# Performance work log

Hardware: AMD Instinct MI355X
Metric: run time of the kernel (lower is better)

Reference implementation:

```python
import jax, jax.numpy as jnp
import numpy as np

RADIUS = 3       # corr_radius
NUM_LEVELS = 4   # corr_lvls


def avg_pool2(x):
    """2x2 avg-pool with stride 2 on the last two axes (floor semantics, like F.avg_pool2d)."""
    nd = x.ndim
    s = jax.lax.reduce_window(
        x, 0.0, jax.lax.add,
        window_dimensions=(1,) * (nd - 2) + (2, 2),
        window_strides=(1,) * (nd - 2) + (2, 2),
        padding='VALID')
    return s * 0.25


def bilinear_window_lookup(corr, coords, radius):
    """corr: [B,H,W,hl,wl] per-pixel correlation maps; coords: [B,H,W,2] (x,y) in
    level-pixel units. Samples a (2r+1)^2 window around each coord with bilinear
    interpolation and zero padding (matches grid_sample align_corners=True, zeros).
    Returns [B,H,W,(2r+1)^2]."""
    B, H, W, hl, wl = corr.shape
    r = radius
    d = jnp.arange(-r, r + 1, dtype=coords.dtype)
    dy, dx = jnp.meshgrid(d, d, indexing='ij')
    delta = jnp.stack([dx.ravel(), dy.ravel()], axis=-1)        # [K2,2] (x,y)
    pts = coords[:, :, :, None, :] + delta                       # [B,H,W,K2,2]
    x, y = pts[..., 0], pts[..., 1]
    x0 = jnp.floor(x); y0 = jnp.floor(y)
    x1 = x0 + 1.0;     y1 = y0 + 1.0
    wx1 = x - x0; wx0 = 1.0 - wx1
    wy1 = y - y0; wy0 = 1.0 - wy1
    bi = jnp.arange(B)[:, None, None, None]
    hi = jnp.arange(H)[None, :, None, None]
    wi = jnp.arange(W)[None, None, :, None]

    def gather(xc, yc):
        valid = (xc >= 0) & (xc <= wl - 1) & (yc >= 0) & (yc <= hl - 1)
        xi = jnp.clip(xc, 0, wl - 1).astype(jnp.int32)
        yi = jnp.clip(yc, 0, hl - 1).astype(jnp.int32)
        return corr[bi, hi, wi, yi, xi] * valid.astype(corr.dtype)

    return (gather(x0, y0) * wx0 * wy0 + gather(x1, y0) * wx1 * wy0 +
            gather(x0, y1) * wx0 * wy1 + gather(x1, y1) * wx1 * wy1)


def pyramid_lookup(pyr, coords, radius):
    """pyr: list of [B,H,W,hl,wl]; coords: [B,H,W,2] at full level-0 resolution.
    Returns [B, L*(2r+1)^2, H, W]."""
    outs = [bilinear_window_lookup(c, coords / float(2 ** lvl), radius)
            for lvl, c in enumerate(pyr)]
    out = jnp.concatenate(outs, axis=-1)
    return jnp.transpose(out, (0, 3, 1, 2))


def setup_inputs() -> dict:
    key = jax.random.key(0)
    k0, k1, k2, k3, k4 = jax.random.split(key, 5)
    B, D, H, W = 1, 128, 60, 108  # 1/8-res features of a padded 480x864 frame
    fmap0 = jax.random.normal(k0, (B, D, H, W), dtype=jnp.float32)
    fmap1 = jax.random.normal(k1, (B, D, H, W), dtype=jnp.float32)
    flow0 = jax.random.normal(k2, (B, 2, H, W), dtype=jnp.float32)
    flow1 = jax.random.normal(k3, (B, 2, H, W), dtype=jnp.float32)
    embt = jax.random.uniform(k4, (B, 1, 1, 1), dtype=jnp.float32,
                              minval=0.1, maxval=0.9)
    return {"fmap0": fmap0, "fmap1": fmap1, "flow0": flow0,
            "flow1": flow1, "embt": embt}


def reference(fmap0, fmap1, flow0, flow1, embt):
    """BidirCorrBlock construction + AMT._corr_scale_lookup (downsample=1).
    Returns [B, 2*L*(2r+1)^2 + 4, H, W]: bidirectional multi-level correlation
    features concatenated with the stacked flows (corr, flow of the torch code)."""
    B, D, H, W = fmap0.shape
    # all-pairs correlation volume, scaled by 1/sqrt(D) as in RAFT's CorrBlock
    corr = jnp.einsum('bchw,bcuv->bhwuv', fmap0, fmap1) / jnp.sqrt(
        jnp.asarray(D, fmap0.dtype))                       # [B,H,W,H,W]
    corr_T = jnp.transpose(corr, (0, 3, 4, 1, 2))          # reversed direction
    pyr, pyr_T = [corr], [corr_T]
    for _ in range(NUM_LEVELS - 1):
        pyr.append(avg_pool2(pyr[-1]))
        pyr_T.append(avg_pool2(pyr_T[-1]))

    # coords_grid: channels (x, y)
    ys, xs = jnp.meshgrid(jnp.arange(H, dtype=fmap0.dtype),
                          jnp.arange(W, dtype=fmap0.dtype), indexing='ij')
    coord = jnp.broadcast_to(jnp.stack([xs, ys], axis=-1), (B, H, W, 2))

    t1_scale = 1.0 / embt           # [B,1,1,1]
    t0_scale = 1.0 / (1.0 - embt)
    f0 = jnp.transpose(flow0, (0, 2, 3, 1))  # [B,H,W,2]
    f1 = jnp.transpose(flow1, (0, 2, 3, 1))
    coords0 = coord + f1 * t1_scale          # lookup args of corr_fn(...)
    coords1 = coord + f0 * t0_scale

    corr0 = pyramid_lookup(pyr, coords0, RADIUS)     # [B, L*K2, H, W]
    corr1 = pyramid_lookup(pyr_T, coords1, RADIUS)
    corr_out = jnp.concatenate([corr0, corr1], axis=1)
    flow_out = jnp.concatenate([flow0, flow1], axis=1)
    return jnp.concatenate([corr_out, flow_out], axis=1)
```

## Files before the change

### kernel.cpp

```cpp
#include <hip/hip_runtime.h>

typedef _Float16 h16;
typedef __attribute__((ext_vector_type(2))) h16 h2v;
typedef __attribute__((ext_vector_type(8))) h16 h8v;

constexpr int H_ = 60, W_ = 108, HW_ = 6480;

constexpr unsigned B_F0T  = 0;
constexpr unsigned B_F1T  = 1658880;
constexpr unsigned B_F0L1 = 3317760;
constexpr unsigned B_F0L2 = 3732480;
constexpr unsigned B_F0L3 = 3836160;
constexpr unsigned B_F1L1 = 3859456;
constexpr unsigned B_F1L2 = 4274176;
constexpr unsigned B_F1L3 = 4377856;

__global__ __launch_bounds__(256) void k_transpose(const float* __restrict__ f0,
                                                   const float* __restrict__ f1,
                                                   h16* __restrict__ ws) {
    __shared__ float lds[64 * 129];
    const float* src = blockIdx.y ? f1 : f0;
    h16* dst = (h16*)((char*)ws + (blockIdx.y ? B_F1T : B_F0T));
    const int p0 = blockIdx.x * 64;
    const int t  = threadIdx.x;
    const int pr = t & 63, cr = t >> 6;
    #pragma unroll
    for (int cb = 0; cb < 128; cb += 4) {
        int c = cb + cr, p = p0 + pr;
        if (p < HW_) lds[pr * 129 + c] = src[(size_t)c * HW_ + p];
    }
    __syncthreads();
    const int cw = t & 63, pw = t >> 6;
    #pragma unroll
    for (int pb = 0; pb < 64; pb += 4) {
        int p = p0 + pb + pw;
        if (p < HW_) {
            float a = lds[(pb + pw) * 129 + 2 * cw];
            float b = lds[(pb + pw) * 129 + 2 * cw + 1];
            h2v v; v.x = (h16)a; v.y = (h16)b;
            ((h2v*)dst)[(size_t)p * 64 + cw] = v;
        }
    }
}

__global__ __launch_bounds__(256) void k_pool(h16* __restrict__ wsh,
                                              int win, int hout, int wout,
                                              unsigned iA, unsigned oA,
                                              unsigned iB, unsigned oB) {
    char* ws = (char*)wsh;
    const unsigned off_in  = blockIdx.y ? iB : iA;
    const unsigned off_out = blockIdx.y ? oB : oA;
    const int idx = blockIdx.x * 256 + threadIdx.x;
    const int total = hout * wout * 16;
    if (idx >= total) return;
    const int pos = idx >> 4, q = idx & 15;
    const int y = pos / wout, x = pos - y * wout;
    const char* r0 = ws + off_in + (unsigned)(2 * y * win + 2 * x) * 256;
    const char* r2 = ws + off_in + (unsigned)((2 * y + 1) * win + 2 * x) * 256;
    h8v a = *(const h8v*)(r0 + q * 16);
    h8v b = *(const h8v*)(r0 + 256 + q * 16);
    h8v c = *(const h8v*)(r2 + q * 16);
    h8v d = *(const h8v*)(r2 + 256 + q * 16);
    h8v o;
    #pragma unroll
    for (int j = 0; j < 8; ++j)
        o[j] = (h16)((((float)a[j] + (float)b[j]) + ((float)c[j] + (float)d[j])) * 0.25f);
    *(h8v*)(ws + off_out + (unsigned)pos * 256 + q * 16) = o;
}

template <int CTRL>
__device__ __forceinline__ float dpp_add(float x) {
    int y = __builtin_amdgcn_update_dpp(0, __builtin_bit_cast(int, x),
                                        CTRL, 0xF, 0xF, true);
    return x + __builtin_bit_cast(float, y);
}

__device__ __forceinline__ float dot_u4(uint4 u, uint4 s, float acc) {
    acc = __builtin_amdgcn_fdot2(__builtin_bit_cast(h2v, u.x),
                                 __builtin_bit_cast(h2v, s.x), acc, false);
    acc = __builtin_amdgcn_fdot2(__builtin_bit_cast(h2v, u.y),
                                 __builtin_bit_cast(h2v, s.y), acc, false);
    acc = __builtin_amdgcn_fdot2(__builtin_bit_cast(h2v, u.z),
                                 __builtin_bit_cast(h2v, s.z), acc, false);
    acc = __builtin_amdgcn_fdot2(__builtin_bit_cast(h2v, u.w),
                                 __builtin_bit_cast(h2v, s.w), acc, false);
    return acc;
}

__global__ __launch_bounds__(256, 4) void k_lookup(const h16* __restrict__ wsh,
                                                   const float* __restrict__ flow0,
                                                   const float* __restrict__ flow1,
                                                   const float* __restrict__ embt,
                                                   float* __restrict__ out) {
    __shared__ float so[196][5];
    const char* ws = (const char*)wsh;
    const int bid = blockIdx.x;
    const int xcd = bid & 7;
    const int dir = xcd >> 2;
    const int ord = (xcd & 3) * 405 + (bid >> 3);
    const int pix0 = ord * 4;
    const int t = threadIdx.x;
    const int L = t & 63;
    const int pix = pix0 + (t >> 6);
    const int h = pix / 108, w = pix - h * 108;

    const float e = embt[0];
    const float scale = dir ? 1.0f / (1.0f - e) : 1.0f / e;
    const float* fl = dir ? flow0 : flow1;
    const float cx = (float)w + fl[pix] * scale;
    const float cy = (float)h + fl[HW_ + pix] * scale;

    const int ch = L & 7;
    const int p  = L >> 3;

    const unsigned sbase = (dir ? B_F1T : B_F0T) + (unsigned)pix * 256;
    uint4 su0 = *(const uint4*)(ws + sbase + ch * 16);
    uint4 su1 = *(const uint4*)(ws + sbase + 128 + ch * 16);
    {
        h8v a = __builtin_bit_cast(h8v, su0), b = __builtin_bit_cast(h8v, su1);
        #pragma unroll
        for (int k = 0; k < 8; ++k) {
            a[k] = a[k] * (h16)0.08838834764831845f;
            b[k] = b[k] * (h16)0.08838834764831845f;
        }
        su0 = __builtin_bit_cast(uint4, a);
        su1 = __builtin_bit_cast(uint4, b);
    }

    constexpr unsigned g0[4] = {B_F1T, B_F1L1, B_F1L2, B_F1L3};
    constexpr unsigned g1[4] = {B_F0T, B_F0L1, B_F0L2, B_F0L3};

    #pragma unroll
    for (int lvl = 0; lvl < 4; ++lvl) {
        const unsigned gbase = dir ? g1[lvl] : g0[lvl];
        const int wl = 108 >> lvl, hl = 60 >> lvl;
        const float inv = (lvl == 0) ? 1.f : (lvl == 1) ? 0.5f : (lvl == 2) ? 0.25f : 0.125f;
        const float cxl = cx * inv, cyl = cy * inv;
        const float bxf = floorf(cxl), byf = floorf(cyl);
        const int bx = (int)bxf, by = (int)byf;
        const int gx = bx - 3 + p;
        const int gxc = min(max(gx, 0), wl - 1);
        const bool colv = (gx >= 0) & (gx < wl);
        const int gyo = by - 3 + ch;
        const bool ownv = colv & (gyo >= 0) & (gyo < hl);

        const unsigned coloff = gbase + (unsigned)gxc * 256 + (unsigned)ch * 16;
        uint4 u0[8], u1[8];
        #pragma unroll
        for (int j = 0; j < 8; ++j) {
            const int gy = by - 3 + j;
            const int gyc = min(max(gy, 0), hl - 1);
            const unsigned ro = coloff + (unsigned)(gyc * wl) * 256;
            u0[j] = *(const uint4*)(ws + ro);
            u1[j] = *(const uint4*)(ws + ro + 128);
        }

        float dval = 0.0f;
        #pragma unroll
        for (int j = 0; j < 8; ++j) {
            float a0 = dot_u4(u0[j], su0, 0.0f);
            float a1 = dot_u4(u1[j], su1, 0.0f);
            float acc = a0 + a1;
            acc = dpp_add<0xB1>(acc);
            acc = dpp_add<0x4E>(acc);
            acc = dpp_add<0x141>(acc);
            dval = (ch == j) ? acc : dval;
        }
        dval = ownv ? dval : 0.0f;

        const int dyi = L / 7, dxi = L - dyi * 7;
        const float fx = cxl - bxf, fy = cyl - byf;
        const float d00 = __shfl(dval, 8 * dxi + dyi);
        const float d01 = __shfl(dval, 8 * dxi + dyi + 8);
        const float d10 = __shfl(dval, 8 * dxi + dyi + 1);
        const float d11 = __shfl(dval, 8 * dxi + dyi + 9);
        const float v = (d00 * (1.0f - fx) + d01 * fx) * (1.0f - fy) +
                        (d10 * (1.0f - fx) + d11 * fx) * fy;
        if (L < 49) so[lvl * 49 + L][t >> 6] = v;
    }
    __syncthreads();

    if (t < 196) {
        float4 o = make_float4(so[t][0], so[t][1], so[t][2], so[t][3]);
        *(float4*)(out + (size_t)(dir * 196 + t) * HW_ + pix0) = o;
    } else if (dir == 0 && t < 200) {
        const int c = t - 196;
        const float* f = (c < 2) ? flow0 + (size_t)c * HW_
                                 : flow1 + (size_t)(c - 2) * HW_;
        *(float4*)(out + (size_t)(392 + c) * HW_ + pix0) = *(const float4*)(f + pix0);
    }
}

extern "C" void kernel_launch(void* const* d_in, const int* in_sizes, int n_in,
                              void* d_out, int out_size, void* d_ws, size_t ws_size,
                              hipStream_t stream) {
    const float* fmap0 = (const float*)d_in[0];
    const float* fmap1 = (const float*)d_in[1];
    const float* flow0 = (const float*)d_in[2];
    const float* flow1 = (const float*)d_in[3];
    const float* embt  = (const float*)d_in[4];
    h16* ws  = (h16*)d_ws;
    float* out = (float*)d_out;

    k_transpose<<<dim3(102, 2), 256, 0, stream>>>(fmap0, fmap1, ws);
    k_pool<<<dim3(102, 2), 256, 0, stream>>>(ws, 108, 30, 54, B_F0T,  B_F0L1, B_F1T,  B_F1L1);
    k_pool<<<dim3(26, 2),  256, 0, stream>>>(ws,  54, 15, 27, B_F0L1, B_F0L2, B_F1L1, B_F1L2);
    k_pool<<<dim3(6, 2),   256, 0, stream>>>(ws,  27,  7, 13, B_F0L2, B_F0L3, B_F1L2, B_F1L3);
    k_lookup<<<dim3(405 * 8), 256, 0, stream>>>(ws, flow0, flow1, embt, out);
}
```

Baseline: 47.55 us.

## Fuse three pooling launches into one kernel computing all pyramid levels from level 0

Replaces the three sequential pooling kernels with a single launch whose block ranges compute levels 1, 2 and 3 directly from the full-resolution transposed features, using 4x4 and 8x8 averages. This removes two kernel launches and the serial dependency between levels. The cost is redundant reads of level 0 for the coarser levels. Averaging in float before a single rounding changes the numerics slightly compared with chained fp16 pooling.

New measurement: 44.62 us. -6.2%, faster.

```diff
diff --git a/kernel.cpp b/kernel.cpp
--- a/kernel.cpp
+++ b/kernel.cpp
@@ -43,29 +43,77 @@
     }
 }
 
-__global__ __launch_bounds__(256) void k_pool(h16* __restrict__ wsh,
-                                              int win, int hout, int wout,
-                                              unsigned iA, unsigned oA,
-                                              unsigned iB, unsigned oB) {
+__global__ __launch_bounds__(256) void k_pyramid(h16* __restrict__ wsh) {
     char* ws = (char*)wsh;
-    const unsigned off_in  = blockIdx.y ? iB : iA;
-    const unsigned off_out = blockIdx.y ? oB : oA;
-    const int idx = blockIdx.x * 256 + threadIdx.x;
-    const int total = hout * wout * 16;
-    if (idx >= total) return;
-    const int pos = idx >> 4, q = idx & 15;
-    const int y = pos / wout, x = pos - y * wout;
-    const char* r0 = ws + off_in + (unsigned)(2 * y * win + 2 * x) * 256;
-    const char* r2 = ws + off_in + (unsigned)((2 * y + 1) * win + 2 * x) * 256;
-    h8v a = *(const h8v*)(r0 + q * 16);
-    h8v b = *(const h8v*)(r0 + 256 + q * 16);
-    h8v c = *(const h8v*)(r2 + q * 16);
-    h8v d = *(const h8v*)(r2 + 256 + q * 16);
-    h8v o;
-    #pragma unroll
-    for (int j = 0; j < 8; ++j)
-        o[j] = (h16)((((float)a[j] + (float)b[j]) + ((float)c[j] + (float)d[j])) * 0.25f);
-    *(h8v*)(ws + off_out + (unsigned)pos * 256 + q * 16) = o;
+    const int map = blockIdx.y;
+    const unsigned srcB = map ? B_F1T : B_F0T;
+    const char* s = ws + srcB;
+    const int bid = blockIdx.x;
+    const int t = threadIdx.x;
+
+    if (bid < 102) {
+        const int idx = bid * 256 + t;
+        if (idx >= 1620 * 16) return;
+        const int pos = idx >> 4, q = idx & 15;
+        const int y = pos / 54, x = pos - y * 54;
+        const unsigned r0 = (unsigned)(2 * y * 108 + 2 * x) * 256 + q * 16;
+        const unsigned r1 = r0 + 108 * 256;
+        h8v a = *(const h8v*)(s + r0);
+        h8v b = *(const h8v*)(s + r0 + 256);
+        h8v c = *(const h8v*)(s + r1);
+        h8v d = *(const h8v*)(s + r1 + 256);
+        h8v o;
+        #pragma unroll
+        for (int k = 0; k < 8; ++k)
+            o[k] = (h16)((((float)a[k] + (float)b[k]) + ((float)c[k] + (float)d[k])) * 0.25f);
+        *(h8v*)(ws + (map ? B_F1L1 : B_F0L1) + (unsigned)pos * 256 + q * 16) = o;
+    } else if (bid < 128) {
+        const int idx = (bid - 102) * 256 + t;
+        if (idx >= 405 * 16) return;
+        const int pos = idx >> 4, q = idx & 15;
+        const int y = pos / 27, x = pos - y * 27;
+        float acc[8] = {};
+        #pragma unroll
+        for (int dy = 0; dy < 4; ++dy) {
+            #pragma unroll
+            for (int dx = 0; dx < 4; ++dx) {
+                h8v u = *(const h8v*)(s + (unsigned)((4 * y + dy) * 108 + 4 * x + dx) * 256 + q * 16);
+                #pragma unroll
+                for (int k = 0; k < 8; ++k) acc[k] += (float)u[k];
+            }
+        }
+        h8v o;
+        #pragma unroll
+        for (int k = 0; k < 8; ++k) o[k] = (h16)(acc[k] * 0.0625f);
+        *(h8v*)(ws + (map ? B_F1L2 : B_F0L2) + (unsigned)pos * 256 + q * 16) = o;
+    } else {
+        const int idx = (bid - 128) * 256 + t;
+        if (idx >= 91 * 128) return;
+        const int pos = idx >> 7;
+        const int sub = idx & 127;
+        const int half = sub >> 6, lane = sub & 63;
+        const int j = lane >> 3, qq = (lane & 7) + half * 8;
+        const int y = pos / 13, x = pos - y * 13;
+        float acc[8] = {};
+        #pragma unroll
+        for (int dx = 0; dx < 8; ++dx) {
+            h8v u = *(const h8v*)(s + (unsigned)((8 * y + j) * 108 + 8 * x + dx) * 256 + qq * 16);
+            #pragma unroll
+            for (int k = 0; k < 8; ++k) acc[k] += (float)u[k];
+        }
+        #pragma unroll
+        for (int k = 0; k < 8; ++k) {
+            acc[k] += __shfl_xor(acc[k], 8);
+            acc[k] += __shfl_xor(acc[k], 16);
+            acc[k] += __shfl_xor(acc[k], 32);
+        }
+        if (j == 0) {
+            h8v o;
+            #pragma unroll
+            for (int k = 0; k < 8; ++k) o[k] = (h16)(acc[k] * 0.015625f);
+            *(h8v*)(ws + (map ? B_F1L3 : B_F0L3) + (unsigned)pos * 256 + qq * 16) = o;
+        }
+    }
 }
 
 template <int CTRL>
@@ -203,8 +251,6 @@
     float* out = (float*)d_out;
 
     k_transpose<<<dim3(102, 2), 256, 0, stream>>>(fmap0, fmap1, ws);
-    k_pool<<<dim3(102, 2), 256, 0, stream>>>(ws, 108, 30, 54, B_F0T,  B_F0L1, B_F1T,  B_F1L1);
-    k_pool<<<dim3(26, 2),  256, 0, stream>>>(ws,  54, 15, 27, B_F0L1, B_F0L2, B_F1L1, B_F1L2);
-    k_pool<<<dim3(6, 2),   256, 0, stream>>>(ws,  27,  7, 13, B_F0L2, B_F0L3, B_F1L2, B_F1L3);
+    k_pyramid<<<dim3(174, 2), 256, 0, stream>>>(ws);
     k_lookup<<<dim3(405 * 8), 256, 0, stream>>>(ws, flow0, flow1, embt, out);
 }
```
